# Kernel optimization log

Hardware: AMD Instinct MI355X
Metric: run time of the kernel (lower is better)

Reference implementation:

```python
import jax, jax.numpy as jnp
import numpy as np

B, N, D = 8, 2048, 512


def setup_inputs() -> dict:
    key = jax.random.key(0)
    ks = jax.random.split(key, 8)
    s = 1.0 / np.sqrt(D)
    return {
        "x": jax.random.normal(ks[0], (B, N, D), dtype=jnp.float32),
        "event_lengths": jax.random.randint(ks[1], (B,), 1, N + 1, dtype=jnp.int64),
        "Wq": jax.random.uniform(ks[2], (D, D), jnp.float32, -s, s),
        "bq": jnp.zeros((D,), jnp.float32),
        "Wk": jax.random.uniform(ks[3], (D, D), jnp.float32, -s, s),
        "bk": jnp.zeros((D,), jnp.float32),
        "Wv": jax.random.uniform(ks[4], (D, D), jnp.float32, -s, s),
        "bv": jnp.zeros((D,), jnp.float32),
    }


def reference(x, event_lengths, Wq, bq, Wk, bk, Wv, bv):
    # x: [B, N, D]; linear layers follow torch convention y = x @ W^T + b
    q = jnp.einsum("bnd,ed->bne", x, Wq) + bq
    k = jnp.einsum("bnd,ed->bne", x, Wk) + bk
    v = jnp.einsum("bnd,ed->bne", x, Wv) + bv

    d = x.shape[-1]
    scores = jnp.einsum("bqd,bkd->bqk", q, k) / jnp.sqrt(jnp.asarray(d, jnp.float32))

    # per-sample padding mask: valid iff row < len AND col < len
    n = x.shape[1]
    idx = jnp.arange(n)
    L = event_lengths[:, None, None]  # [B,1,1]
    mask = (idx[None, :, None] < L) & (idx[None, None, :] < L)  # [B,N,N]
    scores = jnp.where(mask, scores, jnp.float32(-1e9))

    attn = jax.nn.softmax(scores, axis=-1)  # dropout omitted (eval mode)
    return jnp.einsum("bqk,bkd->bqd", attn, v)
```

## Files before the change

kernel.cpp:

```cpp
#include <hip/hip_runtime.h>

typedef _Float16 half8 __attribute__((ext_vector_type(8)));
typedef _Float16 half4 __attribute__((ext_vector_type(4)));
typedef float    floatx4 __attribute__((ext_vector_type(4)));
typedef float    float4v __attribute__((ext_vector_type(4)));

#define BB 8
#define NN 2048
#define DD 512


__device__ __forceinline__ void stage_tile(const _Float16* __restrict__ g,
                                           int gstride, _Float16* lds,
                                           int w, int lane)
{
#pragma unroll
    for (int j = 0; j < 2; ++j) {
        int grp = w * 2 + j;
        int r   = grp * 16 + (lane >> 2);
        int cb  = (lane & 3) ^ ((r >> 1) & 3);
        const _Float16* gp = g + (size_t)r * gstride + cb * 8;
        _Float16* lp = lds + grp * 512;
        __builtin_amdgcn_global_load_lds(
            (const __attribute__((address_space(1))) void*)gp,
            (__attribute__((address_space(3))) void*)lp, 16, 0, 0);
    }
}

__device__ __forceinline__ void stage_tile64(const _Float16* __restrict__ g,
                                             int gstride, _Float16* lds,
                                             int w, int lane)
{
    int r  = w * 16 + (lane >> 2);
    int cb = (lane & 3) ^ ((r >> 1) & 3);
    const _Float16* gp = g + (size_t)r * gstride + cb * 8;
    _Float16* lp = lds + w * 512;
    __builtin_amdgcn_global_load_lds(
        (const __attribute__((address_space(1))) void*)gp,
        (__attribute__((address_space(3))) void*)lp, 16, 0, 0);
}

__device__ __forceinline__ half8 frag(const _Float16* tile, int m, int quad)
{
    return *(const half8*)&tile[m * 32 + ((quad ^ ((m >> 1) & 3)) * 8)];
}

__global__ __launch_bounds__(256) void prep_kernel(
    const float* __restrict__ x, const float* __restrict__ Wq,
    const float* __restrict__ Wk, const float* __restrict__ Wv,
    const int* __restrict__ lens,
    _Float16* __restrict__ xh, _Float16* __restrict__ wqh,
    _Float16* __restrict__ wkh, _Float16* __restrict__ wvh)
{
    const int XQ = (BB * NN * DD) / 4;
    const int WQ = (DD * DD) / 4;
    int t = blockIdx.x * 256 + threadIdx.x;
    const float* src; _Float16* dst; int i;
    if (t < XQ) {
        int row = t >> 7;
        int b   = row >> 11;
        if ((row & 2047) >= ((lens[b] + 127) & ~127)) return;
        src = x;  dst = xh;  i = t;
    }
    else if (t < XQ + WQ)   { src = Wq; dst = wqh; i = t - XQ; }
    else if (t < XQ + 2*WQ) { src = Wk; dst = wkh; i = t - XQ - WQ; }
    else if (t < XQ + 3*WQ) { src = Wv; dst = wvh; i = t - XQ - 2*WQ; }
    else return;
    float4v f = *(const float4v*)&src[(size_t)i * 4];
    half4 h;
    for (int j = 0; j < 4; ++j) h[j] = (_Float16)f[j];
    *(half4*)&dst[(size_t)i * 4] = h;
}

__global__ __launch_bounds__(256) void meanx_kernel(
    const float* __restrict__ x, float* __restrict__ sx)
{
    const int b  = blockIdx.y;
    const int n0 = blockIdx.x * 64;
    const int d0 = threadIdx.x;
    float s0 = 0.f, s1 = 0.f;
    const float* base = x + ((size_t)b * NN + n0) * DD;
    for (int n = 0; n < 64; ++n) {
        s0 += base[n * DD + d0];
        s1 += base[n * DD + d0 + 256];
    }
    atomicAdd(&sx[b * DD + d0], s0);
    atomicAdd(&sx[b * DD + d0 + 256], s1);
}

__global__ __launch_bounds__(256) void mvgemv_kernel(
    const float* __restrict__ Wv, const float* __restrict__ bv,
    const float* __restrict__ sx, float* __restrict__ mean_v)
{
    const int blk = blockIdx.x;
    const int b   = blk >> 7;
    const int e   = (blk & 127) * 4 + (threadIdx.x >> 6);
    const int lane = threadIdx.x & 63;
    const float* wr = Wv + (size_t)e * DD + lane * 8;
    const float* xr = sx + b * DD + lane * 8;
    float s = 0.f;
    for (int j = 0; j < 8; ++j) s += wr[j] * xr[j];
    for (int off = 32; off > 0; off >>= 1) s += __shfl_xor(s, off);
    if (lane == 0)
        mean_v[b * DD + e] = s * (1.0f / 2048.0f) + bv[e];
}

__global__ __launch_bounds__(256) void projqk_kernel(
    const _Float16* __restrict__ xh,
    const _Float16* __restrict__ wqh, const _Float16* __restrict__ wkh,
    const float* __restrict__ bq, const float* __restrict__ bk,
    const int* __restrict__ lens,
    _Float16* __restrict__ qb, _Float16* __restrict__ kb)
{
    const int z = blockIdx.z;
    const int r0 = blockIdx.y * 128;
    const int bb = r0 >> 11;
    if ((r0 & 2047) >= lens[bb]) return;
    const _Float16* Wh  = z ? wkh : wqh;
    const float*    bias= z ? bk  : bq;
    _Float16*       outp= z ? kb  : qb;
    const int c0 = blockIdx.x * 128;

    __shared__ __align__(16) _Float16 As[128 * 32];
    __shared__ __align__(16) _Float16 Bs[128 * 32];

    const int tid  = threadIdx.x;
    const int lane = tid & 63;
    const int w    = tid >> 6;
    const int wm   = w >> 1, wn = w & 1;
    const int lr   = lane & 15;
    const int quad = lane >> 4;

    floatx4 zero; zero[0]=0.f; zero[1]=0.f; zero[2]=0.f; zero[3]=0.f;
    floatx4 acc[4][4];
    for (int i = 0; i < 4; ++i)
        for (int j = 0; j < 4; ++j) acc[i][j] = zero;

    for (int kt = 0; kt < DD / 32; ++kt) {
        __syncthreads();
        stage_tile(xh + (size_t)r0 * DD + kt * 32, DD, As, w, lane);
        stage_tile(Wh + (size_t)c0 * DD + kt * 32, DD, Bs, w, lane);
        __syncthreads();
        half8 a[4], b[4];
        for (int mt = 0; mt < 4; ++mt) a[mt] = frag(As, wm * 64 + mt * 16 + lr, quad);
        for (int nt = 0; nt < 4; ++nt) b[nt] = frag(Bs, wn * 64 + nt * 16 + lr, quad);
        for (int mt = 0; mt < 4; ++mt)
            for (int nt = 0; nt < 4; ++nt)
                acc[mt][nt] = __builtin_amdgcn_mfma_f32_16x16x32_f16(a[mt], b[nt], acc[mt][nt], 0, 0, 0);
    }

    for (int mt = 0; mt < 4; ++mt)
        for (int nt = 0; nt < 4; ++nt)
            for (int r = 0; r < 4; ++r) {
                int row = r0 + wm * 64 + mt * 16 + quad * 4 + r;
                int col = c0 + wn * 64 + nt * 16 + lr;
                outp[(size_t)row * DD + col] = (_Float16)(acc[mt][nt][r] + bias[col]);
            }
}

__global__ __launch_bounds__(256) void projv_kernel(
    const _Float16* __restrict__ xh,
    const _Float16* __restrict__ wvh, const float* __restrict__ bv,
    const int* __restrict__ lens, _Float16* __restrict__ vhT)
{
    const int b  = blockIdx.z;
    const int e0 = blockIdx.y * 128;
    const int n0 = blockIdx.x * 128;
    if (n0 >= lens[b]) return;

    __shared__ __align__(16) _Float16 As[128 * 32];
    __shared__ __align__(16) _Float16 Bs[128 * 32];

    const int tid  = threadIdx.x;
    const int lane = tid & 63;
    const int w    = tid >> 6;
    const int wm   = w >> 1, wn = w & 1;
    const int lr   = lane & 15;
    const int quad = lane >> 4;

    floatx4 zero; zero[0]=0.f; zero[1]=0.f; zero[2]=0.f; zero[3]=0.f;
    floatx4 acc[4][4];
    for (int i = 0; i < 4; ++i)
        for (int j = 0; j < 4; ++j) acc[i][j] = zero;

    for (int kt = 0; kt < DD / 32; ++kt) {
        __syncthreads();
        stage_tile(wvh + (size_t)e0 * DD + kt * 32, DD, As, w, lane);
        stage_tile(xh + ((size_t)b * NN + n0) * DD + kt * 32, DD, Bs, w, lane);
        __syncthreads();
        half8 a[4], bfr[4];
        for (int mt = 0; mt < 4; ++mt) a[mt]   = frag(As, wm * 64 + mt * 16 + lr, quad);
        for (int nt = 0; nt < 4; ++nt) bfr[nt] = frag(Bs, wn * 64 + nt * 16 + lr, quad);
        for (int mt = 0; mt < 4; ++mt)
            for (int nt = 0; nt < 4; ++nt)
                acc[mt][nt] = __builtin_amdgcn_mfma_f32_16x16x32_f16(a[mt], bfr[nt], acc[mt][nt], 0, 0, 0);
    }

    for (int mt = 0; mt < 4; ++mt)
        for (int nt = 0; nt < 4; ++nt)
            for (int r = 0; r < 4; ++r) {
                int e = e0 + wm * 64 + mt * 16 + quad * 4 + r;
                int n = n0 + wn * 64 + nt * 16 + lr;
                vhT[((size_t)b * DD + e) * NN + n] = (_Float16)(acc[mt][nt][r] + bv[e]);
            }
}

__global__ __launch_bounds__(256) void scores_kernel(
    const _Float16* __restrict__ qb, const _Float16* __restrict__ kb,
    const int* __restrict__ lens, _Float16* __restrict__ S)
{
    const int b  = blockIdx.z;
    const int r0 = blockIdx.y * 128;
    const int c0 = blockIdx.x * 128;
    const int L  = lens[b];
    if (r0 >= L || c0 >= L) return;
    const _Float16* A  = qb + (size_t)b * NN * DD;
    const _Float16* Bm = kb + (size_t)b * NN * DD;

    __shared__ __align__(16) _Float16 As[128 * 32];
    __shared__ __align__(16) _Float16 Bs[128 * 32];

    const int tid  = threadIdx.x;
    const int lane = tid & 63;
    const int w    = tid >> 6;
    const int wm   = w >> 1, wn = w & 1;
    const int lr   = lane & 15;
    const int quad = lane >> 4;

    floatx4 zero; zero[0]=0.f; zero[1]=0.f; zero[2]=0.f; zero[3]=0.f;
    floatx4 acc[4][4];
    for (int i = 0; i < 4; ++i)
        for (int j = 0; j < 4; ++j) acc[i][j] = zero;

    for (int kt = 0; kt < DD / 32; ++kt) {
        __syncthreads();
        stage_tile(A  + (size_t)r0 * DD + kt * 32, DD, As, w, lane);
        stage_tile(Bm + (size_t)c0 * DD + kt * 32, DD, Bs, w, lane);
        __syncthreads();
        half8 a[4], bfr[4];
        for (int mt = 0; mt < 4; ++mt) a[mt]   = frag(As, wm * 64 + mt * 16 + lr, quad);
        for (int nt = 0; nt < 4; ++nt) bfr[nt] = frag(Bs, wn * 64 + nt * 16 + lr, quad);
        for (int mt = 0; mt < 4; ++mt)
            for (int nt = 0; nt < 4; ++nt)
                acc[mt][nt] = __builtin_amdgcn_mfma_f32_16x16x32_f16(a[mt], bfr[nt], acc[mt][nt], 0, 0, 0);
    }

    const float scale = 0.044194173824159216f;
    for (int mt = 0; mt < 4; ++mt)
        for (int nt = 0; nt < 4; ++nt)
            for (int r = 0; r < 4; ++r) {
                int q    = r0 + wm * 64 + mt * 16 + quad * 4 + r;
                int kcol = c0 + wn * 64 + nt * 16 + lr;
                S[((size_t)b * NN + q) * NN + kcol] = (_Float16)(acc[mt][nt][r] * scale);
            }
}

__global__ __launch_bounds__(256) void softmax_kernel(
    _Float16* __restrict__ S, const int* __restrict__ lens)
{
    const int b = blockIdx.y, q = blockIdx.x;
    const int L = lens[b];
    if (q >= L) return;
    const int Lp32 = (L + 31) & ~31;
    const size_t base = ((size_t)b * NN + q) * NN;
    const int tid  = threadIdx.x;
    const int lane = tid & 63;
    const int w    = tid >> 6;
    const int k0   = tid * 8;
    const bool active = k0 < Lp32;
    const float NEG = -__builtin_huge_valf();

    float f[8];
    if (active) {
        half8 v = *(const half8*)&S[base + k0];
        for (int j = 0; j < 8; ++j) f[j] = (k0 + j < L) ? (float)v[j] : NEG;
    } else {
        for (int j = 0; j < 8; ++j) f[j] = NEG;
    }

    float m = f[0];
    for (int j = 1; j < 8; ++j) m = fmaxf(m, f[j]);
    for (int off = 32; off > 0; off >>= 1) m = fmaxf(m, __shfl_xor(m, off));
    __shared__ float redm[4];
    __shared__ float reds[4];
    if (lane == 0) redm[w] = m;
    __syncthreads();
    m = fmaxf(fmaxf(redm[0], redm[1]), fmaxf(redm[2], redm[3]));

    float e[8], s = 0.f;
    for (int j = 0; j < 8; ++j) { e[j] = __expf(f[j] - m); s += e[j]; }
    for (int off = 32; off > 0; off >>= 1) s += __shfl_xor(s, off);
    if (lane == 0) reds[w] = s;
    __syncthreads();
    s = (reds[0] + reds[1]) + (reds[2] + reds[3]);

    float inv = 1.0f / s;
    if (active) {
        half8 o;
        for (int j = 0; j < 8; ++j) o[j] = (_Float16)(e[j] * inv);
        *(half8*)&S[base + k0] = o;
    }
}

__global__ __launch_bounds__(256) void pv_kernel(
    const _Float16* __restrict__ P, const _Float16* __restrict__ vhT,
    const int* __restrict__ lens, const float* __restrict__ mean_v,
    float* __restrict__ out)
{
    const int b  = blockIdx.z;
    const int L  = lens[b];
    const int r0 = blockIdx.y * 64;
    const int c0 = blockIdx.x * 128;
    const int KT = (r0 < L) ? ((L + 31) >> 5) : 0;
    const _Float16* A  = P   + (size_t)b * NN * NN;
    const _Float16* Vh = vhT + (size_t)b * DD * NN;

    __shared__ __align__(16) _Float16 As[2][64 * 32];
    __shared__ __align__(16) _Float16 Bhs[2][128 * 32];

    const int tid  = threadIdx.x;
    const int lane = tid & 63;
    const int w    = tid >> 6;
    const int lr   = lane & 15;
    const int quad = lane >> 4;

    floatx4 zero; zero[0]=0.f; zero[1]=0.f; zero[2]=0.f; zero[3]=0.f;
    floatx4 acc[4][2];
    for (int i = 0; i < 4; ++i)
        for (int j = 0; j < 2; ++j) acc[i][j] = zero;

    if (KT > 0) {
        stage_tile64(A + (size_t)r0 * NN, NN, As[0], w, lane);
        stage_tile (Vh + (size_t)c0 * NN, NN, Bhs[0], w, lane);
    }
    for (int kt = 0; kt < KT; ++kt) {
        const int cur = kt & 1;
        __syncthreads();
        if (kt + 1 < KT) {
            stage_tile64(A + (size_t)r0 * NN + (kt + 1) * 32, NN, As[cur ^ 1], w, lane);
            stage_tile (Vh + (size_t)c0 * NN + (kt + 1) * 32, NN, Bhs[cur ^ 1], w, lane);
        }
        half8 a[4], bh[2];
        for (int mt = 0; mt < 4; ++mt) a[mt]  = frag(As[cur], mt * 16 + lr, quad);
        for (int nt = 0; nt < 2; ++nt) bh[nt] = frag(Bhs[cur], w * 32 + nt * 16 + lr, quad);
        for (int mt = 0; mt < 4; ++mt)
            for (int nt = 0; nt < 2; ++nt)
                acc[mt][nt] = __builtin_amdgcn_mfma_f32_16x16x32_f16(a[mt], bh[nt], acc[mt][nt], 0, 0, 0);
    }

    float mval[2];
    for (int nt = 0; nt < 2; ++nt)
        mval[nt] = mean_v[b * DD + c0 + w * 32 + nt * 16 + lr];

    for (int mt = 0; mt < 4; ++mt)
        for (int nt = 0; nt < 2; ++nt)
            for (int r = 0; r < 4; ++r) {
                int q = r0 + mt * 16 + quad * 4 + r;
                int e = c0 + w * 32 + nt * 16 + lr;
                float val = (q < L) ? acc[mt][nt][r] : mval[nt];
                out[((size_t)b * NN + q) * DD + e] = val;
            }
}

extern "C" void kernel_launch(void* const* d_in, const int* in_sizes, int n_in,
                              void* d_out, int out_size, void* d_ws, size_t ws_size,
                              hipStream_t stream) {
    const float* x    = (const float*)d_in[0];
    const int*   lens = (const int*)d_in[1];
    const float* Wq   = (const float*)d_in[2];
    const float* bq   = (const float*)d_in[3];
    const float* Wk   = (const float*)d_in[4];
    const float* bk   = (const float*)d_in[5];
    const float* Wv   = (const float*)d_in[6];
    const float* bv   = (const float*)d_in[7];
    float* out = (float*)d_out;

    char* ws = (char*)d_ws;
    const size_t MB = 1024 * 1024;
    _Float16* qb  = (_Float16*)(ws);
    _Float16* kb  = (_Float16*)(ws + 16 * MB);
    _Float16* vh  = (_Float16*)(ws + 32 * MB);
    float*    mv  = (float*)   (ws + 48 * MB);
    float*    sx  = (float*)   (ws + 48 * MB + 64 * 1024);
    _Float16* S   = (_Float16*)(ws + 64 * MB);
    _Float16* xh  = (_Float16*)(ws + 64 * MB);
    _Float16* wqh = (_Float16*)(ws + 80 * MB);
    _Float16* wkh = (_Float16*)(ws + 80 * MB + 512 * 1024);
    _Float16* wvh = (_Float16*)(ws + 81 * MB);

    hipMemsetAsync(sx, 0, BB * DD * sizeof(float), stream);
    prep_kernel  <<<8960, 256, 0, stream>>>(x, Wq, Wk, Wv, lens, xh, wqh, wkh, wvh);
    meanx_kernel <<<dim3(32, 8),     256, 0, stream>>>(x, sx);
    mvgemv_kernel<<<1024,            256, 0, stream>>>(Wv, bv, sx, mv);
    projqk_kernel<<<dim3(4, 128, 2), 256, 0, stream>>>(xh, wqh, wkh, bq, bk, lens, qb, kb);
    projv_kernel <<<dim3(16, 4, 8),  256, 0, stream>>>(xh, wvh, bv, lens, vh);
    scores_kernel<<<dim3(16, 16, 8), 256, 0, stream>>>(qb, kb, lens, S);
    softmax_kernel<<<dim3(2048, 8),  256, 0, stream>>>(S, lens);
    pv_kernel    <<<dim3(4, 32, 8),  256, 0, stream>>>(S, vh, lens, mv, out);
}
```

Baseline: 213.2 us.

## Add multi-stage async LDS prefetch pipelines to GEMM kernels with explicit vmcnt waits

The projection and scores GEMMs move from a single-buffered load-then-compute loop to a three-buffer ring that prefetches tiles two steps ahead with global_load_lds. The PV kernel goes from a double buffer to a four-deep ring. Explicit s_waitcnt vmcnt and s_barrier replace __syncthreads so memory latency overlaps MFMA work. In exchange, LDS use per block grows, which may lower occupancy, and the tail iterations issue redundant reloads of the last tile.

After: 211.6 us. No clear change (-0.7%).

```diff
diff --git a/kernel.cpp b/kernel.cpp
--- a/kernel.cpp
+++ b/kernel.cpp
@@ -9,6 +9,10 @@
 #define NN 2048
 #define DD 512
 
+
+#define WAITV(N)  asm volatile("s_waitcnt vmcnt(" #N ")" ::: "memory")
+#define WAITL0()  asm volatile("s_waitcnt lgkmcnt(0)" ::: "memory")
+#define BARRIER() asm volatile("s_barrier" ::: "memory")
 
 __device__ __forceinline__ void stage_tile(const _Float16* __restrict__ g,
                                            int gstride, _Float16* lds,
@@ -121,8 +125,8 @@
     _Float16*       outp= z ? kb  : qb;
     const int c0 = blockIdx.x * 128;
 
-    __shared__ __align__(16) _Float16 As[128 * 32];
-    __shared__ __align__(16) _Float16 Bs[128 * 32];
+    __shared__ __align__(16) _Float16 As[3][128 * 32];
+    __shared__ __align__(16) _Float16 Bs[3][128 * 32];
 
     const int tid  = threadIdx.x;
     const int lane = tid & 63;
@@ -136,18 +140,33 @@
     for (int i = 0; i < 4; ++i)
         for (int j = 0; j < 4; ++j) acc[i][j] = zero;
 
-    for (int kt = 0; kt < DD / 32; ++kt) {
-        __syncthreads();
-        stage_tile(xh + (size_t)r0 * DD + kt * 32, DD, As, w, lane);
-        stage_tile(Wh + (size_t)c0 * DD + kt * 32, DD, Bs, w, lane);
-        __syncthreads();
+    const _Float16* Abase = xh + (size_t)r0 * DD;
+    const _Float16* Bbase = Wh + (size_t)c0 * DD;
+
+    stage_tile(Abase +  0, DD, As[0], w, lane);
+    stage_tile(Bbase +  0, DD, Bs[0], w, lane);
+    stage_tile(Abase + 32, DD, As[1], w, lane);
+    stage_tile(Bbase + 32, DD, Bs[1], w, lane);
+
+    int cur = 0;
+    for (int kt = 0; kt < 16; ++kt) {
+        int nx = (kt + 2 < 16) ? kt + 2 : 15;
+        int nb = cur + 2; if (nb >= 3) nb -= 3;
+        stage_tile(Abase + nx * 32, DD, As[nb], w, lane);
+        stage_tile(Bbase + nx * 32, DD, Bs[nb], w, lane);
+        WAITV(8);
+        BARRIER();
         half8 a[4], b[4];
-        for (int mt = 0; mt < 4; ++mt) a[mt] = frag(As, wm * 64 + mt * 16 + lr, quad);
-        for (int nt = 0; nt < 4; ++nt) b[nt] = frag(Bs, wn * 64 + nt * 16 + lr, quad);
+        for (int mt = 0; mt < 4; ++mt) a[mt] = frag(As[cur], wm * 64 + mt * 16 + lr, quad);
+        for (int nt = 0; nt < 4; ++nt) b[nt] = frag(Bs[cur], wn * 64 + nt * 16 + lr, quad);
         for (int mt = 0; mt < 4; ++mt)
             for (int nt = 0; nt < 4; ++nt)
                 acc[mt][nt] = __builtin_amdgcn_mfma_f32_16x16x32_f16(a[mt], b[nt], acc[mt][nt], 0, 0, 0);
-    }
+        WAITL0();
+        BARRIER();
+        cur = (cur + 1 == 3) ? 0 : cur + 1;
+    }
+    WAITV(0);
 
     for (int mt = 0; mt < 4; ++mt)
         for (int nt = 0; nt < 4; ++nt)
@@ -168,8 +187,8 @@
     const int n0 = blockIdx.x * 128;
     if (n0 >= lens[b]) return;
 
-    __shared__ __align__(16) _Float16 As[128 * 32];
-    __shared__ __align__(16) _Float16 Bs[128 * 32];
+    __shared__ __align__(16) _Float16 As[3][128 * 32];
+    __shared__ __align__(16) _Float16 Bs[3][128 * 32];
 
     const int tid  = threadIdx.x;
     const int lane = tid & 63;
@@ -183,18 +202,33 @@
     for (int i = 0; i < 4; ++i)
         for (int j = 0; j < 4; ++j) acc[i][j] = zero;
 
-    for (int kt = 0; kt < DD / 32; ++kt) {
-        __syncthreads();
-        stage_tile(wvh + (size_t)e0 * DD + kt * 32, DD, As, w, lane);
-        stage_tile(xh + ((size_t)b * NN + n0) * DD + kt * 32, DD, Bs, w, lane);
-        __syncthreads();
+    const _Float16* Abase = wvh + (size_t)e0 * DD;
+    const _Float16* Bbase = xh + ((size_t)b * NN + n0) * DD;
+
+    stage_tile(Abase +  0, DD, As[0], w, lane);
+    stage_tile(Bbase +  0, DD, Bs[0], w, lane);
+    stage_tile(Abase + 32, DD, As[1], w, lane);
+    stage_tile(Bbase + 32, DD, Bs[1], w, lane);
+
+    int cur = 0;
+    for (int kt = 0; kt < 16; ++kt) {
+        int nx = (kt + 2 < 16) ? kt + 2 : 15;
+        int nb = cur + 2; if (nb >= 3) nb -= 3;
+        stage_tile(Abase + nx * 32, DD, As[nb], w, lane);
+        stage_tile(Bbase + nx * 32, DD, Bs[nb], w, lane);
+        WAITV(8);
+        BARRIER();
         half8 a[4], bfr[4];
-        for (int mt = 0; mt < 4; ++mt) a[mt]   = frag(As, wm * 64 + mt * 16 + lr, quad);
-        for (int nt = 0; nt < 4; ++nt) bfr[nt] = frag(Bs, wn * 64 + nt * 16 + lr, quad);
+        for (int mt = 0; mt < 4; ++mt) a[mt]   = frag(As[cur], wm * 64 + mt * 16 + lr, quad);
+        for (int nt = 0; nt < 4; ++nt) bfr[nt] = frag(Bs[cur], wn * 64 + nt * 16 + lr, quad);
         for (int mt = 0; mt < 4; ++mt)
             for (int nt = 0; nt < 4; ++nt)
                 acc[mt][nt] = __builtin_amdgcn_mfma_f32_16x16x32_f16(a[mt], bfr[nt], acc[mt][nt], 0, 0, 0);
-    }
+        WAITL0();
+        BARRIER();
+        cur = (cur + 1 == 3) ? 0 : cur + 1;
+    }
+    WAITV(0);
 
     for (int mt = 0; mt < 4; ++mt)
         for (int nt = 0; nt < 4; ++nt)
@@ -214,11 +248,11 @@
     const int c0 = blockIdx.x * 128;
     const int L  = lens[b];
     if (r0 >= L || c0 >= L) return;
-    const _Float16* A  = qb + (size_t)b * NN * DD;
-    const _Float16* Bm = kb + (size_t)b * NN * DD;
-
-    __shared__ __align__(16) _Float16 As[128 * 32];
-    __shared__ __align__(16) _Float16 Bs[128 * 32];
+    const _Float16* Abase = qb + (size_t)b * NN * DD + (size_t)r0 * DD;
+    const _Float16* Bbase = kb + (size_t)b * NN * DD + (size_t)c0 * DD;
+
+    __shared__ __align__(16) _Float16 As[3][128 * 32];
+    __shared__ __align__(16) _Float16 Bs[3][128 * 32];
 
     const int tid  = threadIdx.x;
     const int lane = tid & 63;
@@ -232,18 +266,30 @@
     for (int i = 0; i < 4; ++i)
         for (int j = 0; j < 4; ++j) acc[i][j] = zero;
 
-    for (int kt = 0; kt < DD / 32; ++kt) {
-        __syncthreads();
-        stage_tile(A  + (size_t)r0 * DD + kt * 32, DD, As, w, lane);
-        stage_tile(Bm + (size_t)c0 * DD + kt * 32, DD, Bs, w, lane);
-        __syncthreads();
+    stage_tile(Abase +  0, DD, As[0], w, lane);
+    stage_tile(Bbase +  0, DD, Bs[0], w, lane);
+    stage_tile(Abase + 32, DD, As[1], w, lane);
+    stage_tile(Bbase + 32, DD, Bs[1], w, lane);
+
+    int cur = 0;
+    for (int kt = 0; kt < 16; ++kt) {
+        int nx = (kt + 2 < 16) ? kt + 2 : 15;
+        int nb = cur + 2; if (nb >= 3) nb -= 3;
+        stage_tile(Abase + nx * 32, DD, As[nb], w, lane);
+        stage_tile(Bbase + nx * 32, DD, Bs[nb], w, lane);
+        WAITV(8);
+        BARRIER();
         half8 a[4], bfr[4];
-        for (int mt = 0; mt < 4; ++mt) a[mt]   = frag(As, wm * 64 + mt * 16 + lr, quad);
-        for (int nt = 0; nt < 4; ++nt) bfr[nt] = frag(Bs, wn * 64 + nt * 16 + lr, quad);
+        for (int mt = 0; mt < 4; ++mt) a[mt]   = frag(As[cur], wm * 64 + mt * 16 + lr, quad);
+        for (int nt = 0; nt < 4; ++nt) bfr[nt] = frag(Bs[cur], wn * 64 + nt * 16 + lr, quad);
         for (int mt = 0; mt < 4; ++mt)
             for (int nt = 0; nt < 4; ++nt)
                 acc[mt][nt] = __builtin_amdgcn_mfma_f32_16x16x32_f16(a[mt], bfr[nt], acc[mt][nt], 0, 0, 0);
-    }
+        WAITL0();
+        BARRIER();
+        cur = (cur + 1 == 3) ? 0 : cur + 1;
+    }
+    WAITV(0);
 
     const float scale = 0.044194173824159216f;
     for (int mt = 0; mt < 4; ++mt)
@@ -312,11 +358,11 @@
     const int r0 = blockIdx.y * 64;
     const int c0 = blockIdx.x * 128;
     const int KT = (r0 < L) ? ((L + 31) >> 5) : 0;
-    const _Float16* A  = P   + (size_t)b * NN * NN;
-    const _Float16* Vh = vhT + (size_t)b * DD * NN;
-
-    __shared__ __align__(16) _Float16 As[2][64 * 32];
-    __shared__ __align__(16) _Float16 Bhs[2][128 * 32];
+    const _Float16* A  = P   + (size_t)b * NN * NN + (size_t)r0 * NN;
+    const _Float16* Vh = vhT + (size_t)b * DD * NN + (size_t)c0 * NN;
+
+    __shared__ __align__(16) _Float16 As[4][64 * 32];
+    __shared__ __align__(16) _Float16 Bhs[4][128 * 32];
 
     const int tid  = threadIdx.x;
     const int lane = tid & 63;
@@ -330,22 +376,30 @@
         for (int j = 0; j < 2; ++j) acc[i][j] = zero;
 
     if (KT > 0) {
-        stage_tile64(A + (size_t)r0 * NN, NN, As[0], w, lane);
-        stage_tile (Vh + (size_t)c0 * NN, NN, Bhs[0], w, lane);
-    }
-    for (int kt = 0; kt < KT; ++kt) {
-        const int cur = kt & 1;
-        __syncthreads();
-        if (kt + 1 < KT) {
-            stage_tile64(A + (size_t)r0 * NN + (kt + 1) * 32, NN, As[cur ^ 1], w, lane);
-            stage_tile (Vh + (size_t)c0 * NN + (kt + 1) * 32, NN, Bhs[cur ^ 1], w, lane);
+        for (int i = 0; i < 3; ++i) {
+            int t0 = (i < KT) ? i : KT - 1;
+            stage_tile64(A  + t0 * 32, NN, As[i],  w, lane);
+            stage_tile (Vh + t0 * 32, NN, Bhs[i], w, lane);
         }
-        half8 a[4], bh[2];
-        for (int mt = 0; mt < 4; ++mt) a[mt]  = frag(As[cur], mt * 16 + lr, quad);
-        for (int nt = 0; nt < 2; ++nt) bh[nt] = frag(Bhs[cur], w * 32 + nt * 16 + lr, quad);
-        for (int mt = 0; mt < 4; ++mt)
-            for (int nt = 0; nt < 2; ++nt)
-                acc[mt][nt] = __builtin_amdgcn_mfma_f32_16x16x32_f16(a[mt], bh[nt], acc[mt][nt], 0, 0, 0);
+        int cur = 0;
+        for (int kt = 0; kt < KT; ++kt) {
+            int nx = (kt + 3 < KT) ? kt + 3 : KT - 1;
+            int nb = cur + 3; if (nb >= 4) nb -= 4;
+            stage_tile64(A  + nx * 32, NN, As[nb],  w, lane);
+            stage_tile (Vh + nx * 32, NN, Bhs[nb], w, lane);
+            WAITV(9);
+            BARRIER();
+            half8 a[4], bh[2];
+            for (int mt = 0; mt < 4; ++mt) a[mt]  = frag(As[cur], mt * 16 + lr, quad);
+            for (int nt = 0; nt < 2; ++nt) bh[nt] = frag(Bhs[cur], w * 32 + nt * 16 + lr, quad);
+            for (int mt = 0; mt < 4; ++mt)
+                for (int nt = 0; nt < 2; ++nt)
+                    acc[mt][nt] = __builtin_amdgcn_mfma_f32_16x16x32_f16(a[mt], bh[nt], acc[mt][nt], 0, 0, 0);
+            WAITL0();
+            BARRIER();
+            cur = (cur + 1 == 4) ? 0 : cur + 1;
+        }
+        WAITV(0);
     }
 
     float mval[2];
```
